# Optimization experiments

Measured on AMD Instinct MI355X. Metric: run time of the kernel, lower is better.

The kernel has to match this reference:

```python
import jax, jax.numpy as jnp
import numpy as np

BUCKET_SIZE = 64  # must divide seq_len


def setup_inputs() -> dict:
    key = jax.random.key(0)
    k1, k2, k3, k4 = jax.random.split(key, 4)
    B, S, D = 4, 4096, 1024
    query = jax.random.normal(k1, (B, S, D), dtype=jnp.float32)
    key_t = jax.random.normal(k2, (B, S, D), dtype=jnp.float32)
    value = jax.random.normal(k3, (B, S, D), dtype=jnp.float32)
    # random hashing hyperplanes: [B, D, bucket_size // 2]
    R = jax.random.normal(k4, (B, D, BUCKET_SIZE // 2), dtype=jnp.float32)
    return {"query": query, "key": key_t, "value": value, "R": R}


def reference(query, key, value, R):
    B, S, D = query.shape
    # random projection: [B, S, bucket_size // 2]
    xR = jnp.einsum("bsd,bdr->bsr", query, R)
    # mirror trick -> [B, S, bucket_size]
    concat_xR = jnp.concatenate([xR, -xR], axis=-1)
    buckets = jnp.argmax(concat_xR, axis=-1)          # [B, S] int
    sticker = jnp.argsort(buckets, axis=-1)            # token permutation into buckets
    undo_sort = jnp.argsort(sticker, axis=-1)          # computed in original (unused)
    # batched gather (tf.gather batch_dims=1, axis=1)
    sorted_query = jnp.take_along_axis(query, sticker[..., None], axis=1)
    sorted_value = jnp.take_along_axis(value, sticker[..., None], axis=1)
    # tf.split(x, bucket_size, 1) then stack(axis=1) == reshape to chunks
    chunked_query = sorted_query.reshape(B, BUCKET_SIZE, S // BUCKET_SIZE, D)
    chunked_value = sorted_value.reshape(B, BUCKET_SIZE, S // BUCKET_SIZE, D)
    del undo_sort, chunked_query, chunked_value  # dead code in original; module returns sticker
    return sticker
```

## Files before the change

### kernel.cpp

```cpp
#include <hip/hip_runtime.h>


#define B_DIM 4
#define S_LEN 4096
#define D_DIM 1024
#define NRR 32
#define NBK 64
#define TMK 64
#define NCHUNK (S_LEN / TMK)
#define NKQ 4
#define QOFF 2048
#define PSL 2048

typedef const __attribute__((address_space(1))) void* gas_t;
typedef __attribute__((address_space(3))) void* las_t;

#define FMA4(A, S, B)                                                        \
    (A).x = fmaf((S), (B).x, (A).x); (A).y = fmaf((S), (B).y, (A).y);        \
    (A).z = fmaf((S), (B).z, (A).z); (A).w = fmaf((S), (B).w, (A).w);

__global__ void __launch_bounds__(256) __attribute__((amdgpu_waves_per_eu(2, 2)))
k1_gemm(const float* __restrict__ Q, const float* __restrict__ R,
        float4* __restrict__ P4)
{
    __shared__ float4 smem4[QOFF + 2048];

    const int bid = blockIdx.x;
    const int kqr = bid & 3;
    const int chunk = (bid >> 2) & 63;
    const int b = bid >> 8;

    const int t = threadIdx.x;
    const int w = t >> 6;
    const int lane = t & 63;
    const int tok_t = lane >> 5;
    const int r_t = (lane >> 3) & 3;
    const int kl = lane & 7;

    const float4* Qw4 = (const float4*)(Q + ((size_t)b * S_LEN + chunk * TMK + w * 16) * D_DIM);
    const float4* Rg4 = (const float4*)(R + (size_t)b * D_DIM * NRR);

#define STAGE_R()                                                             \
    {                                                                         \
        _Pragma("unroll")                                                     \
        for (int i = 0; i < 8; ++i) {                                         \
            const int rel = w * 512 + i * 64 + lane;                          \
            const int kh = rel >> 3, v = rel & 7;                             \
            __builtin_amdgcn_global_load_lds(                                 \
                (gas_t)(Rg4 + ((size_t)kqr * 256 + kh) * 8 + (v ^ ((kh >> 3) & 7))), \
                (las_t)&smem4[w * 512 + i * 64], 16, 0, 0);                   \
        }                                                                     \
    }

#define ISSUE_Q(TILE, DST)                                                    \
    {                                                                         \
        _Pragma("unroll")                                                     \
        for (int i = 0; i < 4; ++i) {                                         \
            const int f = i * 64 + lane;                                      \
            const int td = f >> 4, sd = f & 15;                               \
            __builtin_amdgcn_global_load_lds(                                 \
                (gas_t)(Qw4 + (size_t)td * 256 + kqr * 64 + (TILE) * 16       \
                        + (sd ^ (td >> 3))),                                  \
                (las_t)&smem4[QOFF + w * 512 + (DST) * 256 + i * 64], 16, 0, 0);\
        }                                                                     \
    }

#define COMPUTE(TILE, BUF)                                                    \
    {                                                                         \
        const float4* qb = smem4 + QOFF + w * 512 + (BUF) * 256;              \
        const float4* rb = smem4;                                             \
        _Pragma("unroll")                                                     \
        for (int kap = 0; kap < 2; ++kap) {                                   \
            float4 qv[8];                                                     \
            _Pragma("unroll")                                                 \
            for (int j = 0; j < 8; ++j)                                       \
                qv[j] = qb[(tok_t * 8 + j) * 16 + (((kl << 1) + kap) ^ tok_t)];\
            _Pragma("unroll")                                                 \
            for (int c = 0; c < 4; ++c) {                                     \
                const int krow = (TILE) * 64 + kl * 8 + kap * 4 + c;          \
                const float4 rv0 = rb[krow * 8 + ((r_t * 2 + 0) ^ kl)];       \
                const float4 rv1 = rb[krow * 8 + ((r_t * 2 + 1) ^ kl)];       \
                _Pragma("unroll")                                             \
                for (int j = 0; j < 8; ++j) {                                 \
                    const float s = c == 0 ? qv[j].x : c == 1 ? qv[j].y       \
                                  : c == 2 ? qv[j].z : qv[j].w;               \
                    FMA4(acc[j][0], s, rv0);                                  \
                    FMA4(acc[j][1], s, rv1);                                  \
                }                                                             \
            }                                                                 \
        }                                                                     \
    }

    float4 acc[8][2];
#pragma unroll
    for (int j = 0; j < 8; ++j) {
        acc[j][0] = make_float4(0.f, 0.f, 0.f, 0.f);
        acc[j][1] = make_float4(0.f, 0.f, 0.f, 0.f);
    }

    STAGE_R()
    ISSUE_Q(0, 0)
    asm volatile("s_waitcnt vmcnt(0)" ::: "memory");
    __syncthreads();

#pragma unroll
    for (int tau = 0; tau < 4; ++tau) {
        if (tau + 1 < 4) {
            asm volatile("s_waitcnt lgkmcnt(0)" ::: "memory");
            ISSUE_Q(tau + 1, (tau + 1) & 1)
        }
        COMPUTE(tau, tau & 1)
        asm volatile("s_waitcnt vmcnt(0)" ::: "memory");
    }
#undef STAGE_R
#undef ISSUE_Q
#undef COMPUTE

#pragma unroll
    for (int j = 0; j < 8; ++j)
#pragma unroll
        for (int p = 0; p < 2; ++p)
#pragma unroll
            for (int off = 1; off < 8; off <<= 1) {
                acc[j][p].x += __shfl_xor(acc[j][p].x, off, 64);
                acc[j][p].y += __shfl_xor(acc[j][p].y, off, 64);
                acc[j][p].z += __shfl_xor(acc[j][p].z, off, 64);
                acc[j][p].w += __shfl_xor(acc[j][p].w, off, 64);
            }

    if (kl == 0) {
        float4* Pb = P4 + (((size_t)b * NCHUNK + chunk) * NKQ + kqr) * (PSL / 4);
#pragma unroll
        for (int j = 0; j < 8; ++j) {
            const int tok = w * 16 + tok_t * 8 + j;
            Pb[tok * 8 + r_t * 2 + 0] = acc[j][0];
            Pb[tok * 8 + r_t * 2 + 1] = acc[j][1];
        }
    }
}

__global__ __launch_bounds__(256) void k1c_combine(
    const float* __restrict__ P,
    int* __restrict__ buckets, int* __restrict__ hist)
{
    __shared__ float xs[TMK][NRR + 1];
    __shared__ int cnt[NBK];

    const int bid = blockIdx.x;
    const int b = bid >> 6;
    const int h = bid & 63;
    const int t = threadIdx.x;

    const float* Pb = P + ((size_t)b * NCHUNK + h) * NKQ * PSL;
#pragma unroll
    for (int i = 0; i < 8; ++i) {
        const int idx = t + 256 * i;
        const int tok = idx >> 5, r = idx & 31;
        const size_t base = (size_t)tok * NRR + r;
        xs[tok][r] = Pb[base] + Pb[base + PSL] + Pb[base + 2 * PSL] + Pb[base + 3 * PSL];
    }
    if (t < NBK) cnt[t] = 0;
    __syncthreads();

    if (t < TMK) {
        float m1 = xs[t][0]; int i1 = 0;
        float m2 = m1;       int i2 = 0;
#pragma unroll
        for (int r = 1; r < NRR; ++r) {
            const float v = xs[t][r];
            if (v > m1) { m1 = v; i1 = r; }
            if (v < m2) { m2 = v; i2 = r; }
        }
        const int bk = (m1 >= -m2) ? i1 : (NRR + i2);
        buckets[(size_t)b * S_LEN + h * TMK + t] = bk;
        atomicAdd(&cnt[bk], 1);
    }
    __syncthreads();
    if (t < NBK) hist[((size_t)b * NCHUNK + h) * NBK + t] = cnt[t];
}

__global__ __launch_bounds__(256) void k2_scan(
    const int* __restrict__ hist, int* __restrict__ chunkOffset)
{
    const int t = threadIdx.x;
    const int b = t >> 6;
    const int bk = t & 63;
    const int lane = t & 63;

    int total = 0;
    for (int c = 0; c < NCHUNK; ++c)
        total += hist[((size_t)b * NCHUNK + c) * NBK + bk];

    int incl = total;
#pragma unroll
    for (int off = 1; off < 64; off <<= 1) {
        int n = __shfl_up(incl, off, 64);
        if (lane >= off) incl += n;
    }
    int run = incl - total;

    for (int c = 0; c < NCHUNK; ++c) {
        int h = hist[((size_t)b * NCHUNK + c) * NBK + bk];
        chunkOffset[((size_t)b * NCHUNK + c) * NBK + bk] = run;
        run += h;
    }
}

__global__ __launch_bounds__(256) void k3_scatter(
    const int* __restrict__ buckets, const int* __restrict__ chunkOffset,
    int* __restrict__ out)
{
    const int gid = blockIdx.x * 256 + threadIdx.x;
    const int b = gid >> 12;
    const int s = gid & (S_LEN - 1);
    const int chunk = s >> 6;
    const int lane = threadIdx.x & 63;

    const int bk = buckets[gid];

    unsigned long long m = ~0ull;
#pragma unroll
    for (int i = 0; i < 6; ++i) {
        unsigned long long bi = __ballot((bk >> i) & 1);
        m &= ((bk >> i) & 1) ? bi : ~bi;
    }
    int rank = __popcll(m & ((1ull << lane) - 1ull));

    int pos = chunkOffset[((size_t)b * NCHUNK + chunk) * NBK + bk] + rank;
    out[(size_t)b * S_LEN + pos] = s;
}

extern "C" void kernel_launch(void* const* d_in, const int* in_sizes, int n_in,
                              void* d_out, int out_size, void* d_ws, size_t ws_size,
                              hipStream_t stream) {
    const float* Q = (const float*)d_in[0];
    const float* R = (const float*)d_in[3];

    float* P         = (float*)d_ws;
    int* buckets     = (int*)(P + (size_t)B_DIM * NCHUNK * NKQ * PSL);
    int* hist        = buckets + B_DIM * S_LEN;
    int* chunkOffset = hist + B_DIM * NCHUNK * NBK;

    k1_gemm    <<<B_DIM * NCHUNK * NKQ, 256, 0, stream>>>(Q, R, (float4*)P);
    k1c_combine<<<B_DIM * NCHUNK,       256, 0, stream>>>(P, buckets, hist);
    k2_scan    <<<1,                    256, 0, stream>>>(hist, chunkOffset);
    k3_scatter <<<(B_DIM * S_LEN) / 256, 256, 0, stream>>>(buckets, chunkOffset, (int*)d_out);
}
```

Baseline: 41.03 us.

## Split GEMM reduction dimension 16 ways and drop in-block tile pipeline

The projection GEMM now splits the D reduction into 16 slices instead of 4. Each block loads a single 64-wide K tile of Q and R and computes it without the double-buffered loop. This quadruples the grid to 4096 blocks, shrinks shared memory and raises the waves-per-EU hint to 4, aiming for more parallelism and latency hiding. The cost is 4x more partial-sum traffic: the combine kernel must now read and add 16 partials per element instead of 4.

```diff
diff --git a/kernel.cpp b/kernel.cpp
--- a/kernel.cpp
+++ b/kernel.cpp
@@ -8,8 +8,8 @@
 #define NBK 64
 #define TMK 64
 #define NCHUNK (S_LEN / TMK)
-#define NKQ 4
-#define QOFF 2048
+#define NKS 16
+#define QOFF 512
 #define PSL 2048
 
 typedef const __attribute__((address_space(1))) void* gas_t;
@@ -19,16 +19,16 @@
     (A).x = fmaf((S), (B).x, (A).x); (A).y = fmaf((S), (B).y, (A).y);        \
     (A).z = fmaf((S), (B).z, (A).z); (A).w = fmaf((S), (B).w, (A).w);
 
-__global__ void __launch_bounds__(256) __attribute__((amdgpu_waves_per_eu(2, 2)))
+__global__ void __launch_bounds__(256) __attribute__((amdgpu_waves_per_eu(4, 4)))
 k1_gemm(const float* __restrict__ Q, const float* __restrict__ R,
         float4* __restrict__ P4)
 {
-    __shared__ float4 smem4[QOFF + 2048];
+    __shared__ float4 smem4[QOFF + 1024];
 
     const int bid = blockIdx.x;
-    const int kqr = bid & 3;
-    const int chunk = (bid >> 2) & 63;
-    const int b = bid >> 8;
+    const int ks = bid & 15;
+    const int chunk = (bid >> 4) & 63;
+    const int b = bid >> 10;
 
     const int t = threadIdx.x;
     const int w = t >> 6;
@@ -36,60 +36,30 @@
     const int tok_t = lane >> 5;
     const int r_t = (lane >> 3) & 3;
     const int kl = lane & 7;
+    const int rsw0 = (r_t * 2 + 0) ^ kl;
+    const int rsw1 = (r_t * 2 + 1) ^ kl;
 
     const float4* Qw4 = (const float4*)(Q + ((size_t)b * S_LEN + chunk * TMK + w * 16) * D_DIM);
     const float4* Rg4 = (const float4*)(R + (size_t)b * D_DIM * NRR);
 
-#define STAGE_R()                                                             \
-    {                                                                         \
-        _Pragma("unroll")                                                     \
-        for (int i = 0; i < 8; ++i) {                                         \
-            const int rel = w * 512 + i * 64 + lane;                          \
-            const int kh = rel >> 3, v = rel & 7;                             \
-            __builtin_amdgcn_global_load_lds(                                 \
-                (gas_t)(Rg4 + ((size_t)kqr * 256 + kh) * 8 + (v ^ ((kh >> 3) & 7))), \
-                (las_t)&smem4[w * 512 + i * 64], 16, 0, 0);                   \
-        }                                                                     \
-    }
-
-#define ISSUE_Q(TILE, DST)                                                    \
-    {                                                                         \
-        _Pragma("unroll")                                                     \
-        for (int i = 0; i < 4; ++i) {                                         \
-            const int f = i * 64 + lane;                                      \
-            const int td = f >> 4, sd = f & 15;                               \
-            __builtin_amdgcn_global_load_lds(                                 \
-                (gas_t)(Qw4 + (size_t)td * 256 + kqr * 64 + (TILE) * 16       \
-                        + (sd ^ (td >> 3))),                                  \
-                (las_t)&smem4[QOFF + w * 512 + (DST) * 256 + i * 64], 16, 0, 0);\
-        }                                                                     \
-    }
-
-#define COMPUTE(TILE, BUF)                                                    \
-    {                                                                         \
-        const float4* qb = smem4 + QOFF + w * 512 + (BUF) * 256;              \
-        const float4* rb = smem4;                                             \
-        _Pragma("unroll")                                                     \
-        for (int kap = 0; kap < 2; ++kap) {                                   \
-            float4 qv[8];                                                     \
-            _Pragma("unroll")                                                 \
-            for (int j = 0; j < 8; ++j)                                       \
-                qv[j] = qb[(tok_t * 8 + j) * 16 + (((kl << 1) + kap) ^ tok_t)];\
-            _Pragma("unroll")                                                 \
-            for (int c = 0; c < 4; ++c) {                                     \
-                const int krow = (TILE) * 64 + kl * 8 + kap * 4 + c;          \
-                const float4 rv0 = rb[krow * 8 + ((r_t * 2 + 0) ^ kl)];       \
-                const float4 rv1 = rb[krow * 8 + ((r_t * 2 + 1) ^ kl)];       \
-                _Pragma("unroll")                                             \
-                for (int j = 0; j < 8; ++j) {                                 \
-                    const float s = c == 0 ? qv[j].x : c == 1 ? qv[j].y       \
-                                  : c == 2 ? qv[j].z : qv[j].w;               \
-                    FMA4(acc[j][0], s, rv0);                                  \
-                    FMA4(acc[j][1], s, rv1);                                  \
-                }                                                             \
-            }                                                                 \
-        }                                                                     \
-    }
+#pragma unroll
+    for (int i = 0; i < 2; ++i) {
+        const int rel = w * 128 + i * 64 + lane;
+        const int kh = rel >> 3, v = rel & 7;
+        __builtin_amdgcn_global_load_lds(
+            (gas_t)(Rg4 + ((size_t)ks * 64 + kh) * 8 + (v ^ ((kh >> 3) & 7))),
+            (las_t)&smem4[w * 128 + i * 64], 16, 0, 0);
+    }
+#pragma unroll
+    for (int i = 0; i < 4; ++i) {
+        const int f = i * 64 + lane;
+        const int td = f >> 4, sd = f & 15;
+        __builtin_amdgcn_global_load_lds(
+            (gas_t)(Qw4 + (size_t)td * 256 + ks * 16 + (sd ^ (td >> 3))),
+            (las_t)&smem4[QOFF + w * 256 + i * 64], 16, 0, 0);
+    }
+    asm volatile("s_waitcnt vmcnt(0)" ::: "memory");
+    __syncthreads();
 
     float4 acc[8][2];
 #pragma unroll
@@ -97,24 +67,30 @@
         acc[j][0] = make_float4(0.f, 0.f, 0.f, 0.f);
         acc[j][1] = make_float4(0.f, 0.f, 0.f, 0.f);
     }
-
-    STAGE_R()
-    ISSUE_Q(0, 0)
-    asm volatile("s_waitcnt vmcnt(0)" ::: "memory");
-    __syncthreads();
-
-#pragma unroll
-    for (int tau = 0; tau < 4; ++tau) {
-        if (tau + 1 < 4) {
-            asm volatile("s_waitcnt lgkmcnt(0)" ::: "memory");
-            ISSUE_Q(tau + 1, (tau + 1) & 1)
-        }
-        COMPUTE(tau, tau & 1)
-        asm volatile("s_waitcnt vmcnt(0)" ::: "memory");
-    }
-#undef STAGE_R
-#undef ISSUE_Q
-#undef COMPUTE
+    const float4* rb = smem4;
+    const float4* qb = smem4 + QOFF + w * 256;
+
+#pragma unroll
+    for (int kap = 0; kap < 2; ++kap) {
+        float4 rv[4][2];
+#pragma unroll
+        for (int c = 0; c < 4; ++c) {
+            const int krow = kl * 8 + kap * 4 + c;
+            rv[c][0] = rb[krow * 8 + rsw0];
+            rv[c][1] = rb[krow * 8 + rsw1];
+        }
+#pragma unroll
+        for (int j = 0; j < 8; ++j) {
+            const float4 qv = qb[(tok_t * 8 + j) * 16 + ((kl * 2 + kap) ^ tok_t)];
+#pragma unroll
+            for (int c = 0; c < 4; ++c) {
+                const float s = c == 0 ? qv.x : c == 1 ? qv.y
+                              : c == 2 ? qv.z : qv.w;
+                FMA4(acc[j][0], s, rv[c][0]);
+                FMA4(acc[j][1], s, rv[c][1]);
+            }
+        }
+    }
 
 #pragma unroll
     for (int j = 0; j < 8; ++j)
@@ -129,7 +105,7 @@
             }
 
     if (kl == 0) {
-        float4* Pb = P4 + (((size_t)b * NCHUNK + chunk) * NKQ + kqr) * (PSL / 4);
+        float4* Pb = P4 + (((size_t)ks * B_DIM + b) * NCHUNK + chunk) * (PSL / 4);
 #pragma unroll
         for (int j = 0; j < 8; ++j) {
             const int tok = w * 16 + tok_t * 8 + j;
@@ -151,13 +127,15 @@
     const int h = bid & 63;
     const int t = threadIdx.x;
 
-    const float* Pb = P + ((size_t)b * NCHUNK + h) * NKQ * PSL;
 #pragma unroll
     for (int i = 0; i < 8; ++i) {
         const int idx = t + 256 * i;
         const int tok = idx >> 5, r = idx & 31;
-        const size_t base = (size_t)tok * NRR + r;
-        xs[tok][r] = Pb[base] + Pb[base + PSL] + Pb[base + 2 * PSL] + Pb[base + 3 * PSL];
+        float s = 0.f;
+#pragma unroll
+        for (int ks = 0; ks < NKS; ++ks)
+            s += P[(((size_t)ks * B_DIM + b) * NCHUNK + h) * PSL + tok * NRR + r];
+        xs[tok][r] = s;
     }
     if (t < NBK) cnt[t] = 0;
     __syncthreads();
@@ -237,11 +215,11 @@
     const float* R = (const float*)d_in[3];
 
     float* P         = (float*)d_ws;
-    int* buckets     = (int*)(P + (size_t)B_DIM * NCHUNK * NKQ * PSL);
+    int* buckets     = (int*)(P + (size_t)NKS * B_DIM * NCHUNK * PSL);
     int* hist        = buckets + B_DIM * S_LEN;
     int* chunkOffset = hist + B_DIM * NCHUNK * NBK;
 
-    k1_gemm    <<<B_DIM * NCHUNK * NKQ, 256, 0, stream>>>(Q, R, (float4*)P);
+    k1_gemm    <<<B_DIM * NCHUNK * NKS, 256, 0, stream>>>(Q, R, (float4*)P);
     k1c_combine<<<B_DIM * NCHUNK,       256, 0, stream>>>(P, buckets, hist);
     k2_scan    <<<1,                    256, 0, stream>>>(hist, chunkOffset);
     k3_scatter <<<(B_DIM * S_LEN) / 256, 256, 0, stream>>>(buckets, chunkOffset, (int*)d_out);
```

Result: slower. 70.92 us (+72.8%).

## Split projection GEMM K-dimension eight ways with triple-buffered Q tiles

Applied to the files above, without the earlier changes.

Doubles the split-K factor of the query-by-hyperplane projection from 4 to 8 slices, doubling the grid size and halving per-block LDS and work. Q tiles now use a three-deep buffer with explicit vmcnt waits instead of a double-buffered loop. The compute loop is reordered to hold R values in registers and stream Q per token. Waves per EU is raised to 4. The combine kernel now sums 8 partials per element, which adds partial-sum traffic and atomic-free reduction work in exchange for more parallelism and occupancy.

```diff
diff --git a/kernel.cpp b/kernel.cpp
--- a/kernel.cpp
+++ b/kernel.cpp
@@ -8,8 +8,8 @@
 #define NBK 64
 #define TMK 64
 #define NCHUNK (S_LEN / TMK)
-#define NKQ 4
-#define QOFF 2048
+#define NKQ 8
+#define QOFF 1024
 #define PSL 2048
 
 typedef const __attribute__((address_space(1))) void* gas_t;
@@ -19,16 +19,16 @@
     (A).x = fmaf((S), (B).x, (A).x); (A).y = fmaf((S), (B).y, (A).y);        \
     (A).z = fmaf((S), (B).z, (A).z); (A).w = fmaf((S), (B).w, (A).w);
 
-__global__ void __launch_bounds__(256) __attribute__((amdgpu_waves_per_eu(2, 2)))
+__global__ void __launch_bounds__(256) __attribute__((amdgpu_waves_per_eu(4, 4)))
 k1_gemm(const float* __restrict__ Q, const float* __restrict__ R,
         float4* __restrict__ P4)
 {
-    __shared__ float4 smem4[QOFF + 2048];
+    __shared__ float4 smem4[QOFF + 1536];
 
     const int bid = blockIdx.x;
-    const int kqr = bid & 3;
-    const int chunk = (bid >> 2) & 63;
-    const int b = bid >> 8;
+    const int kqr = bid & 7;
+    const int chunk = (bid >> 3) & 63;
+    const int b = bid >> 9;
 
     const int t = threadIdx.x;
     const int w = t >> 6;
@@ -43,50 +43,48 @@
 #define STAGE_R()                                                             \
     {                                                                         \
         _Pragma("unroll")                                                     \
-        for (int i = 0; i < 8; ++i) {                                         \
-            const int rel = w * 512 + i * 64 + lane;                          \
-            const int kh = rel >> 3, v = rel & 7;                             \
+        for (int i = 0; i < 4; ++i) {                                         \
+            const int f = w * 256 + i * 64 + lane;                            \
+            const int kh = f >> 3, v = f & 7;                                 \
             __builtin_amdgcn_global_load_lds(                                 \
-                (gas_t)(Rg4 + ((size_t)kqr * 256 + kh) * 8 + (v ^ ((kh >> 3) & 7))), \
-                (las_t)&smem4[w * 512 + i * 64], 16, 0, 0);                   \
+                (gas_t)(Rg4 + ((size_t)kqr * 128 + kh) * 8 + (v ^ ((kh >> 2) & 7))), \
+                (las_t)&smem4[w * 256 + i * 64], 16, 0, 0);                   \
         }                                                                     \
     }
 
 #define ISSUE_Q(TILE, DST)                                                    \
     {                                                                         \
         _Pragma("unroll")                                                     \
-        for (int i = 0; i < 4; ++i) {                                         \
+        for (int i = 0; i < 2; ++i) {                                         \
             const int f = i * 64 + lane;                                      \
-            const int td = f >> 4, sd = f & 15;                               \
+            const int td = f >> 3, sd = f & 7;                                \
             __builtin_amdgcn_global_load_lds(                                 \
-                (gas_t)(Qw4 + (size_t)td * 256 + kqr * 64 + (TILE) * 16       \
+                (gas_t)(Qw4 + (size_t)td * 256 + kqr * 32 + (TILE) * 8        \
                         + (sd ^ (td >> 3))),                                  \
-                (las_t)&smem4[QOFF + w * 512 + (DST) * 256 + i * 64], 16, 0, 0);\
+                (las_t)&smem4[QOFF + w * 384 + (DST) * 128 + i * 64], 16, 0, 0);\
         }                                                                     \
     }
 
 #define COMPUTE(TILE, BUF)                                                    \
     {                                                                         \
-        const float4* qb = smem4 + QOFF + w * 512 + (BUF) * 256;              \
+        const float4* qb = smem4 + QOFF + w * 384 + (BUF) * 128;              \
         const float4* rb = smem4;                                             \
-        _Pragma("unroll")                                                     \
-        for (int kap = 0; kap < 2; ++kap) {                                   \
-            float4 qv[8];                                                     \
-            _Pragma("unroll")                                                 \
-            for (int j = 0; j < 8; ++j)                                       \
-                qv[j] = qb[(tok_t * 8 + j) * 16 + (((kl << 1) + kap) ^ tok_t)];\
+        float4 rv[4][2];                                                      \
+        _Pragma("unroll")                                                     \
+        for (int c = 0; c < 4; ++c) {                                         \
+            const int krow = (TILE) * 32 + kl * 4 + c;                        \
+            rv[c][0] = rb[krow * 8 + ((r_t * 2 + 0) ^ kl)];                   \
+            rv[c][1] = rb[krow * 8 + ((r_t * 2 + 1) ^ kl)];                   \
+        }                                                                     \
+        _Pragma("unroll")                                                     \
+        for (int j = 0; j < 8; ++j) {                                         \
+            const float4 qv = qb[(tok_t * 8 + j) * 8 + (kl ^ tok_t)];         \
             _Pragma("unroll")                                                 \
             for (int c = 0; c < 4; ++c) {                                     \
-                const int krow = (TILE) * 64 + kl * 8 + kap * 4 + c;          \
-                const float4 rv0 = rb[krow * 8 + ((r_t * 2 + 0) ^ kl)];       \
-                const float4 rv1 = rb[krow * 8 + ((r_t * 2 + 1) ^ kl)];       \
-                _Pragma("unroll")                                             \
-                for (int j = 0; j < 8; ++j) {                                 \
-                    const float s = c == 0 ? qv[j].x : c == 1 ? qv[j].y       \
-                                  : c == 2 ? qv[j].z : qv[j].w;               \
-                    FMA4(acc[j][0], s, rv0);                                  \
-                    FMA4(acc[j][1], s, rv1);                                  \
-                }                                                             \
+                const float s = c == 0 ? qv.x : c == 1 ? qv.y                 \
+                              : c == 2 ? qv.z : qv.w;                         \
+                FMA4(acc[j][0], s, rv[c][0]);                                 \
+                FMA4(acc[j][1], s, rv[c][1]);                                 \
             }                                                                 \
         }                                                                     \
     }
@@ -100,18 +98,19 @@
 
     STAGE_R()
     ISSUE_Q(0, 0)
+    ISSUE_Q(1, 1)
     asm volatile("s_waitcnt vmcnt(0)" ::: "memory");
     __syncthreads();
 
-#pragma unroll
-    for (int tau = 0; tau < 4; ++tau) {
-        if (tau + 1 < 4) {
-            asm volatile("s_waitcnt lgkmcnt(0)" ::: "memory");
-            ISSUE_Q(tau + 1, (tau + 1) & 1)
-        }
-        COMPUTE(tau, tau & 1)
-        asm volatile("s_waitcnt vmcnt(0)" ::: "memory");
-    }
+    ISSUE_Q(2, 2)
+    COMPUTE(0, 0)
+    asm volatile("s_waitcnt lgkmcnt(0)" ::: "memory");
+    ISSUE_Q(3, 0)
+    COMPUTE(1, 1)
+    asm volatile("s_waitcnt vmcnt(2)" ::: "memory");
+    COMPUTE(2, 2)
+    asm volatile("s_waitcnt vmcnt(0)" ::: "memory");
+    COMPUTE(3, 0)
 #undef STAGE_R
 #undef ISSUE_Q
 #undef COMPUTE
@@ -157,7 +156,10 @@
         const int idx = t + 256 * i;
         const int tok = idx >> 5, r = idx & 31;
         const size_t base = (size_t)tok * NRR + r;
-        xs[tok][r] = Pb[base] + Pb[base + PSL] + Pb[base + 2 * PSL] + Pb[base + 3 * PSL];
+        float s = 0.f;
+#pragma unroll
+        for (int ks = 0; ks < NKQ; ++ks) s += Pb[base + (size_t)ks * PSL];
+        xs[tok][r] = s;
     }
     if (t < NBK) cnt[t] = 0;
     __syncthreads();
```

New measurement: 69.62 us. 69.7% more time.
